# Performance work log

Hardware: AMD Instinct MI355X
Metric: run time of the kernel (lower is better)

Reference implementation:

```python
import jax, jax.numpy as jnp
import numpy as np

K, S = 8, 4  # patch kernel and stride (overlapping: stride < kernel)


def _patch_idx(H, W):
    nH = (H - K) // S + 1
    nW = (W - K) // S + 1
    hh = (jnp.arange(nH) * S)[:, None] + jnp.arange(K)[None, :]  # [nH, K]
    ww = (jnp.arange(nW) * S)[:, None] + jnp.arange(K)[None, :]  # [nW, K]
    return nH, nW, hh, ww


def _split(x):
    # x: [B, C, H, W] -> [B*N, K*K, C] (same token/patch ordering as nn.Unfold)
    B, C, H, W = x.shape
    nH, nW, hh, ww = _patch_idx(H, W)
    # gather overlapping patches: [B, C, nH, nW, K, K]
    p = x[:, :, hh[:, None, :, None], ww[None, :, None, :]]
    p = jnp.transpose(p, (0, 2, 3, 4, 5, 1))  # [B, nH, nW, K, K, C]
    return p.reshape(B * nH * nW, K * K, C)


def _merge(z, B, C, H, W):
    # z: [B*N, K*K, C] -> overlap-add fold -> [B, C, H, W] (matches nn.Fold)
    nH, nW, hh, ww = _patch_idx(H, W)
    y = z.reshape(B, nH, nW, K, K, C)
    y = jnp.transpose(y, (0, 5, 1, 2, 3, 4))  # [B, C, nH, nW, K, K]
    out = jnp.zeros((B, C, H, W), z.dtype)
    out = out.at[:, :, hh[:, None, :, None], ww[None, :, None, :]].add(y)
    return out


def reference(q, k, v):
    B, C, H, W = v.shape
    qp = _split(q)  # [BN, KK, C]
    kp = _split(k)
    vp = _split(v)
    scale = C ** (-0.5)
    # per-patch attention over KK=64 tokens
    attn = jax.nn.softmax(scale * jnp.einsum('ntc,nsc->nts', qp, kp), axis=-1)
    z = jnp.einsum('nts,nsc->ntc', attn, vp)  # [BN, KK, C]
    return _merge(z, B, C, H, W)


def setup_inputs() -> dict:
    key = jax.random.key(0)
    k1, k2, k3 = jax.random.split(key, 3)
    shape = (8, 128, 128, 128)  # [B, C, H, W]
    return {
        'q': jax.random.normal(k1, shape, dtype=jnp.float32),
        'k': jax.random.normal(k2, shape, dtype=jnp.float32),
        'v': jax.random.normal(k3, shape, dtype=jnp.float32),
    }
```

## Files before the change

### kernel.cpp

```cpp
#include <hip/hip_runtime.h>

#define B_    8
#define C_    128
#define H_    128
#define W_    128
#define NH    31
#define NPB   (NH*NH)
#define NPAT  (B_*NPB)
#define HW_   (H_*W_)
#define CHW_  (C_*HW_)
#define WS_BYTES ((size_t)NPAT * 8192 * 2)

typedef float v4f __attribute__((ext_vector_type(4)));
typedef short v8s __attribute__((ext_vector_type(8)));

__device__ __forceinline__ unsigned short f2bf(float f) {
    unsigned int u = __builtin_bit_cast(unsigned int, f);
    u += 0x7FFFu + ((u >> 16) & 1u);
    return (unsigned short)(u >> 16);
}
__device__ __forceinline__ float bflo(unsigned int d) {
    return __builtin_bit_cast(float, d << 16);
}
__device__ __forceinline__ float bfhi(unsigned int d) {
    return __builtin_bit_cast(float, d & 0xFFFF0000u);
}


__global__ __launch_bounds__(512, 6)
void patch_attn_ws(const float* __restrict__ q,
                   const float* __restrict__ k,
                   const float* __restrict__ v,
                   unsigned short* __restrict__ ws)
{
    __shared__ __align__(16) unsigned char lds[43264];
    unsigned short* sQ   = (unsigned short*)(lds);
    unsigned short* sK   = (unsigned short*)(lds + 16384);
    unsigned short* sVT  = (unsigned short*)(lds);
    unsigned short* sP   = (unsigned short*)(lds + 32768);
    float*          sRedM= (float*)(lds + 40960);
    float*          sRedL= (float*)(lds + 41984);
    float*          sInv = (float*)(lds + 43008);
    unsigned short* sRep = (unsigned short*)(lds);

    const int tid  = threadIdx.x;
    const int lane = tid & 63;
    const int wid  = tid >> 6;
    const int l15  = lane & 15;
    const int quad = lane >> 4;

    const int p   = (blockIdx.x & 7) * NPB + (blockIdx.x >> 3);
    const int b   = p / NPB;
    const int rem = p - b * NPB;
    const int ph  = rem / NH;
    const int pw  = rem - ph * NH;
    const int h0  = ph * 4, w0 = pw * 4;
    const int baseB = b * CHW_;

    float4 rq[4], rk[4], rv[4];
    int cA[4], tA[4];
    #pragma unroll
    for (int g = 0; g < 4; ++g) {
        int flat4 = tid + g * 512;
        int jj = flat4 & 1;
        int i  = (flat4 >> 1) & 7;
        int c  = flat4 >> 4;
        int off = baseB + c * HW_ + (h0 + i) * W_ + (w0 + jj * 4);
        rq[g] = *(const float4*)(q + off);
        rk[g] = *(const float4*)(k + off);
        rv[g] = *(const float4*)(v + off);
        cA[g] = c;
        tA[g] = i * 8 + jj * 4;
    }
    #pragma unroll
    for (int g = 0; g < 4; ++g) {
        const float* fq = (const float*)&rq[g];
        const float* fk = (const float*)&rk[g];
        int c = cA[g];
        #pragma unroll
        for (int d = 0; d < 4; ++d) {
            int t = tA[g] + d;
            int idx = t * 128 + ((((c >> 3) ^ (t & 15)) << 3) | (c & 7));
            sQ[idx] = f2bf(fq[d]);
            sK[idx] = f2bf(fk[d]);
        }
    }
    __syncthreads();

    const float scale = 0.08838834764831845f;
    const int nt  = wid & 3;
    const int mt0 = wid >> 2;

    v4f accT[2];
    #pragma unroll
    for (int ti = 0; ti < 2; ++ti) {
        int mt = mt0 + ti * 2;
        v4f acc = {0.f, 0.f, 0.f, 0.f};
        int rowA = mt * 16 + l15;
        int rowB = nt * 16 + l15;
        #pragma unroll
        for (int kk = 0; kk < 4; ++kk) {
            int gph = (kk * 4 + quad) ^ l15;
            v8s a  = *(const v8s*)(&sQ[rowA * 128 + gph * 8]);
            v8s bb = *(const v8s*)(&sK[rowB * 128 + gph * 8]);
            acc = __builtin_amdgcn_mfma_f32_16x16x32_bf16(a, bb, acc, 0, 0, 0);
        }
        #pragma unroll
        for (int r = 0; r < 4; ++r) acc[r] *= scale;
        accT[ti] = acc;
    }

    float4 mloc[2], eV[2];
    #pragma unroll
    for (int ti = 0; ti < 2; ++ti) {
        float4 m;
        #pragma unroll
        for (int r = 0; r < 4; ++r) m[r] = accT[ti][r];
        #pragma unroll
        for (int mask = 1; mask <= 8; mask <<= 1)
            #pragma unroll
            for (int r = 0; r < 4; ++r) m[r] = fmaxf(m[r], __shfl_xor(m[r], mask));
        float4 e, l;
        #pragma unroll
        for (int r = 0; r < 4; ++r) { e[r] = __expf(accT[ti][r] - m[r]); l[r] = e[r]; }
        #pragma unroll
        for (int mask = 1; mask <= 8; mask <<= 1)
            #pragma unroll
            for (int r = 0; r < 4; ++r) l[r] += __shfl_xor(l[r], mask);
        mloc[ti] = m; eV[ti] = e;
        if (l15 == 0) {
            int tb = (mt0 + ti * 2) * 16 + quad * 4;
            #pragma unroll
            for (int r = 0; r < 4; ++r) {
                sRedM[nt * 64 + tb + r] = m[r];
                sRedL[nt * 64 + tb + r] = l[r];
            }
        }
    }
    __syncthreads();

    #pragma unroll
    for (int g = 0; g < 4; ++g) {
        const float* fv = (const float*)&rv[g];
        unsigned short tmp[4];
        #pragma unroll
        for (int d = 0; d < 4; ++d) tmp[d] = f2bf(fv[d]);
        int c = cA[g], s0 = tA[g];
        int idx = c * 64 + ((((s0 >> 3) ^ (c & 7)) << 3) | (s0 & 7));
        *(uint2*)(&sVT[idx]) = *(const uint2*)tmp;
    }

    #pragma unroll
    for (int ti = 0; ti < 2; ++ti) {
        int tb = (mt0 + ti * 2) * 16 + quad * 4;
        float4 Mv[4], Lv[4];
        #pragma unroll
        for (int n2 = 0; n2 < 4; ++n2) {
            Mv[n2] = *(const float4*)(&sRedM[n2 * 64 + tb]);
            Lv[n2] = *(const float4*)(&sRedL[n2 * 64 + tb]);
        }
        float4 M = Mv[0], L;
        #pragma unroll
        for (int n2 = 1; n2 < 4; ++n2)
            #pragma unroll
            for (int r = 0; r < 4; ++r) M[r] = fmaxf(M[r], Mv[n2][r]);
        #pragma unroll
        for (int r = 0; r < 4; ++r) L[r] = 0.f;
        #pragma unroll
        for (int n2 = 0; n2 < 4; ++n2)
            #pragma unroll
            for (int r = 0; r < 4; ++r) L[r] += Lv[n2][r] * __expf(Mv[n2][r] - M[r]);
        #pragma unroll
        for (int r = 0; r < 4; ++r) {
            float pv = eV[ti][r] * __expf(mloc[ti][r] - M[r]);
            int t = tb + r;
            int s = nt * 16 + l15;
            sP[t * 64 + ((((s >> 3) ^ (t & 7)) << 3) | (s & 7))] = f2bf(pv);
        }
        if (nt == 0 && l15 == 0) {
            #pragma unroll
            for (int r = 0; r < 4; ++r) sInv[tb + r] = 1.0f / L[r];
        }
    }
    __syncthreads();

    v4f z[4];
    #pragma unroll
    for (int n2 = 0; n2 < 4; ++n2) z[n2] = (v4f){0.f, 0.f, 0.f, 0.f};
    const int crow = wid * 16 + l15;
    #pragma unroll
    for (int kk = 0; kk < 2; ++kk) {
        int gph = (kk * 4 + quad) ^ (l15 & 7);
        v8s a = *(const v8s*)(&sVT[crow * 64 + gph * 8]);
        #pragma unroll
        for (int n2 = 0; n2 < 4; ++n2) {
            int trow = n2 * 16 + l15;
            v8s bb = *(const v8s*)(&sP[trow * 64 + gph * 8]);
            z[n2] = __builtin_amdgcn_mfma_f32_16x16x32_bf16(a, bb, z[n2], 0, 0, 0);
        }
    }
    __syncthreads();

    #pragma unroll
    for (int n2 = 0; n2 < 4; ++n2) {
        int t = n2 * 16 + l15;
        float inv = sInv[t];
        #pragma unroll
        for (int r = 0; r < 4; ++r) {
            int c = wid * 16 + quad * 4 + r;
            sRep[c * 70 + t] = f2bf(z[n2][r] * inv);
        }
    }
    __syncthreads();
    {
        int c = tid >> 2, tseg = tid & 3;
        const unsigned short* src = &sRep[c * 70 + tseg * 16];
        uint2 d0 = *(const uint2*)(src);
        uint2 d1 = *(const uint2*)(src + 4);
        uint2 d2 = *(const uint2*)(src + 8);
        uint2 d3 = *(const uint2*)(src + 12);
        unsigned short* dst = ws + (size_t)p * 8192 + c * 64 + tseg * 16;
        uint4 w0v; w0v.x = d0.x; w0v.y = d0.y; w0v.z = d1.x; w0v.w = d1.y;
        uint4 w1v; w1v.x = d2.x; w1v.y = d2.y; w1v.z = d3.x; w1v.w = d3.y;
        ((uint4*)dst)[0] = w0v;
        ((uint4*)dst)[1] = w1v;
    }
}


#define MSLOT 264
#define MARR  (33 * MSLOT)

__global__ __launch_bounds__(256, 4)
void merge_kernel(const unsigned short* __restrict__ ws,
                  float* __restrict__ out)
{
    __shared__ __align__(16) unsigned short sM[2 * MARR];
    unsigned short* sA = sM;
    unsigned short* sB = sM + MARR;

    const int tid  = threadIdx.x;
    const int b    = blockIdx.x & 7;
    const int rest = blockIdx.x >> 3;
    const int hq   = rest >> 4;
    const int cg   = rest & 15;

    if (tid < 132) {
        int target = tid / 33;
        int j      = tid - target * 33;
        unsigned short* base = ((target < 2) ? sA : sB)
                             + ((target & 1) ? 32 * MSLOT : 0);
        uint4 zz; zz.x = 0u; zz.y = 0u; zz.z = 0u; zz.w = 0u;
        *(uint4*)(base + j * 8) = zz;
    }

    const int aValid = (hq <= 30);
    const int bValid = (hq >= 1);
    const int hqB = bValid ? (hq - 1) : 0;
    const size_t rowA = (size_t)(b * NPB + hq  * NH) * 8192;
    const size_t rowB = (size_t)(b * NPB + hqB * NH) * 8192;

    #pragma unroll
    for (int it = 0; it < 8; ++it) {
        int flat = tid + it * 256;
        if (flat < 1984) {
            int half = (flat >= 992);
            int fl   = flat - (half ? 992 : 0);
            int seg  = fl >> 2;
            int sub  = fl & 3;
            int pw   = seg >> 3;
            int csub = seg & 7;
            const unsigned short* src = ws
                + (half ? rowB : rowA)
                + (size_t)pw * 8192
                + (size_t)(cg * 8 + csub) * 64
                + (half ? 32 : 0)
                + sub * 8;
            int valid = half ? bValid : aValid;
            uint4 val;
            if (valid) {
                val = *(const uint4*)src;
            } else {
                val.x = 0u; val.y = 0u; val.z = 0u; val.w = 0u;
            }
            unsigned short* dst = (half ? sB : sA)
                + (pw + 1) * MSLOT + csub * 32 + sub * 8;
            *(uint4*)dst = val;
        }
    }
    __syncthreads();

    const int l    = tid & 31;
    const int csub = tid >> 5;
    const int c    = cg * 8 + csub;

    float* op = out + b * CHW_ + c * HW_ + (hq * 4) * W_ + l * 4;
    #pragma unroll
    for (int hr = 0; hr < 4; ++hr) {
        int baseL = (l + 1) * MSLOT + csub * 32 + hr * 8;
        int baseP = l       * MSLOT + csub * 32 + hr * 8 + 4;
        uint2 aL = *(const uint2*)(sA + baseL);
        uint2 aP = *(const uint2*)(sA + baseP);
        uint2 bL = *(const uint2*)(sB + baseL);
        uint2 bP = *(const uint2*)(sB + baseP);
        float4 r;
        r.x = bflo(aL.x) + bflo(aP.x) + bflo(bL.x) + bflo(bP.x);
        r.y = bfhi(aL.x) + bfhi(aP.x) + bfhi(bL.x) + bfhi(bP.x);
        r.z = bflo(aL.y) + bflo(aP.y) + bflo(bL.y) + bflo(bP.y);
        r.w = bfhi(aL.y) + bfhi(aP.y) + bfhi(bL.y) + bfhi(bP.y);
        *(float4*)(op + hr * W_) = r;
    }
}


__global__ __launch_bounds__(512, 6)
void patch_attn_atomic(const float* __restrict__ q,
                       const float* __restrict__ k,
                       const float* __restrict__ v,
                       float* __restrict__ out)
{
    __shared__ __align__(16) unsigned char lds[43264];
    unsigned short* sQ   = (unsigned short*)(lds);
    unsigned short* sK   = (unsigned short*)(lds + 16384);
    unsigned short* sVT  = (unsigned short*)(lds);
    unsigned short* sP   = (unsigned short*)(lds + 32768);
    float*          sRedM= (float*)(lds + 40960);
    float*          sRedL= (float*)(lds + 41984);
    float*          sInv = (float*)(lds + 43008);

    const int tid  = threadIdx.x;
    const int lane = tid & 63;
    const int wid  = tid >> 6;
    const int l15  = lane & 15;
    const int quad = lane >> 4;

    const int p   = (blockIdx.x & 7) * NPB + (blockIdx.x >> 3);
    const int b   = p / NPB;
    const int rem = p - b * NPB;
    const int ph  = rem / NH;
    const int pw  = rem - ph * NH;
    const int h0  = ph * 4, w0 = pw * 4;
    const int baseB = b * CHW_;

    float4 rq[4], rk[4], rv[4];
    int cA[4], tA[4];
    #pragma unroll
    for (int g = 0; g < 4; ++g) {
        int flat4 = tid + g * 512;
        int jj = flat4 & 1;
        int i  = (flat4 >> 1) & 7;
        int c  = flat4 >> 4;
        int off = baseB + c * HW_ + (h0 + i) * W_ + (w0 + jj * 4);
        rq[g] = *(const float4*)(q + off);
        rk[g] = *(const float4*)(k + off);
        rv[g] = *(const float4*)(v + off);
        cA[g] = c;
        tA[g] = i * 8 + jj * 4;
    }
    #pragma unroll
    for (int g = 0; g < 4; ++g) {
        const float* fq = (const float*)&rq[g];
        const float* fk = (const float*)&rk[g];
        int c = cA[g];
        #pragma unroll
        for (int d = 0; d < 4; ++d) {
            int t = tA[g] + d;
            int idx = t * 128 + ((((c >> 3) ^ (t & 15)) << 3) | (c & 7));
            sQ[idx] = f2bf(fq[d]);
            sK[idx] = f2bf(fk[d]);
        }
    }
    __syncthreads();

    const float scale = 0.08838834764831845f;
    const int nt  = wid & 3;
    const int mt0 = wid >> 2;

    v4f accT[2];
    #pragma unroll
    for (int ti = 0; ti < 2; ++ti) {
        int mt = mt0 + ti * 2;
        v4f acc = {0.f, 0.f, 0.f, 0.f};
        int rowA = mt * 16 + l15;
        int rowB = nt * 16 + l15;
        #pragma unroll
        for (int kk = 0; kk < 4; ++kk) {
            int gph = (kk * 4 + quad) ^ l15;
            v8s a  = *(const v8s*)(&sQ[rowA * 128 + gph * 8]);
            v8s bb = *(const v8s*)(&sK[rowB * 128 + gph * 8]);
            acc = __builtin_amdgcn_mfma_f32_16x16x32_bf16(a, bb, acc, 0, 0, 0);
        }
        #pragma unroll
        for (int r = 0; r < 4; ++r) acc[r] *= scale;
        accT[ti] = acc;
    }

    float4 mloc[2], eV[2];
    #pragma unroll
    for (int ti = 0; ti < 2; ++ti) {
        float4 m;
        #pragma unroll
        for (int r = 0; r < 4; ++r) m[r] = accT[ti][r];
        #pragma unroll
        for (int mask = 1; mask <= 8; mask <<= 1)
            #pragma unroll
            for (int r = 0; r < 4; ++r) m[r] = fmaxf(m[r], __shfl_xor(m[r], mask));
        float4 e, l;
        #pragma unroll
        for (int r = 0; r < 4; ++r) { e[r] = __expf(accT[ti][r] - m[r]); l[r] = e[r]; }
        #pragma unroll
        for (int mask = 1; mask <= 8; mask <<= 1)
            #pragma unroll
            for (int r = 0; r < 4; ++r) l[r] += __shfl_xor(l[r], mask);
        mloc[ti] = m; eV[ti] = e;
        if (l15 == 0) {
            int tb = (mt0 + ti * 2) * 16 + quad * 4;
            #pragma unroll
            for (int r = 0; r < 4; ++r) {
                sRedM[nt * 64 + tb + r] = m[r];
                sRedL[nt * 64 + tb + r] = l[r];
            }
        }
    }
    __syncthreads();

    #pragma unroll
    for (int g = 0; g < 4; ++g) {
        const float* fv = (const float*)&rv[g];
        unsigned short tmp[4];
        #pragma unroll
        for (int d = 0; d < 4; ++d) tmp[d] = f2bf(fv[d]);
        int c = cA[g], s0 = tA[g];
        int idx = c * 64 + ((((s0 >> 3) ^ (c & 7)) << 3) | (s0 & 7));
        *(uint2*)(&sVT[idx]) = *(const uint2*)tmp;
    }

    #pragma unroll
    for (int ti = 0; ti < 2; ++ti) {
        int tb = (mt0 + ti * 2) * 16 + quad * 4;
        float4 Mv[4], Lv[4];
        #pragma unroll
        for (int n2 = 0; n2 < 4; ++n2) {
            Mv[n2] = *(const float4*)(&sRedM[n2 * 64 + tb]);
            Lv[n2] = *(const float4*)(&sRedL[n2 * 64 + tb]);
        }
        float4 M = Mv[0], L;
        #pragma unroll
        for (int n2 = 1; n2 < 4; ++n2)
            #pragma unroll
            for (int r = 0; r < 4; ++r) M[r] = fmaxf(M[r], Mv[n2][r]);
        #pragma unroll
        for (int r = 0; r < 4; ++r) L[r] = 0.f;
        #pragma unroll
        for (int n2 = 0; n2 < 4; ++n2)
            #pragma unroll
            for (int r = 0; r < 4; ++r) L[r] += Lv[n2][r] * __expf(Mv[n2][r] - M[r]);
        #pragma unroll
        for (int r = 0; r < 4; ++r) {
            float pv = eV[ti][r] * __expf(mloc[ti][r] - M[r]);
            int t = tb + r;
            int s = nt * 16 + l15;
            sP[t * 64 + ((((s >> 3) ^ (t & 7)) << 3) | (s & 7))] = f2bf(pv);
        }
        if (nt == 0 && l15 == 0) {
            #pragma unroll
            for (int r = 0; r < 4; ++r) sInv[tb + r] = 1.0f / L[r];
        }
    }
    __syncthreads();

    v4f z[4];
    #pragma unroll
    for (int n2 = 0; n2 < 4; ++n2) z[n2] = (v4f){0.f, 0.f, 0.f, 0.f};
    const int crow = wid * 16 + l15;
    #pragma unroll
    for (int kk = 0; kk < 2; ++kk) {
        int gph = (kk * 4 + quad) ^ (l15 & 7);
        v8s a = *(const v8s*)(&sVT[crow * 64 + gph * 8]);
        #pragma unroll
        for (int n2 = 0; n2 < 4; ++n2) {
            int trow = n2 * 16 + l15;
            v8s bb = *(const v8s*)(&sP[trow * 64 + gph * 8]);
            z[n2] = __builtin_amdgcn_mfma_f32_16x16x32_bf16(a, bb, z[n2], 0, 0, 0);
        }
    }

    #pragma unroll
    for (int n2 = 0; n2 < 4; ++n2) {
        int t = n2 * 16 + l15;
        float inv = sInv[t];
        int base2 = baseB + (h0 + (t >> 3)) * W_ + (w0 + (t & 7));
        #pragma unroll
        for (int r = 0; r < 4; ++r) {
            int c = wid * 16 + quad * 4 + r;
            unsafeAtomicAdd(out + base2 + c * HW_, z[n2][r] * inv);
        }
    }
}

extern "C" void kernel_launch(void* const* d_in, const int* in_sizes, int n_in,
                              void* d_out, int out_size, void* d_ws, size_t ws_size,
                              hipStream_t stream) {
    const float* q = (const float*)d_in[0];
    const float* k = (const float*)d_in[1];
    const float* v = (const float*)d_in[2];
    float* out = (float*)d_out;

    if (ws_size >= WS_BYTES) {
        unsigned short* ws = (unsigned short*)d_ws;
        patch_attn_ws<<<NPAT, 512, 0, stream>>>(q, k, v, ws);
        merge_kernel<<<8 * 32 * 16, 256, 0, stream>>>(ws, out);
    } else {
        hipMemsetAsync(out, 0, (size_t)out_size * sizeof(float), stream);
        patch_attn_atomic<<<NPAT, 512, 0, stream>>>(q, k, v, out);
    }
}
```

Baseline: 350.2 us.

## Restructure patch attention to 4 waves with in-wave softmax and smaller LDS

```diff
diff --git a/kernel.cpp b/kernel.cpp
--- a/kernel.cpp
+++ b/kernel.cpp
@@ -19,6 +19,9 @@
     u += 0x7FFFu + ((u >> 16) & 1u);
     return (unsigned short)(u >> 16);
 }
+__device__ __forceinline__ unsigned int pack2bf(float lo, float hi) {
+    return (unsigned int)f2bf(lo) | ((unsigned int)f2bf(hi) << 16);
+}
 __device__ __forceinline__ float bflo(unsigned int d) {
     return __builtin_bit_cast(float, d << 16);
 }
@@ -27,27 +30,24 @@
 }
 
 
-__global__ __launch_bounds__(512, 6)
+__global__ __launch_bounds__(256, 4)
 void patch_attn_ws(const float* __restrict__ q,
                    const float* __restrict__ k,
                    const float* __restrict__ v,
                    unsigned short* __restrict__ ws)
 {
-    __shared__ __align__(16) unsigned char lds[43264];
-    unsigned short* sQ   = (unsigned short*)(lds);
-    unsigned short* sK   = (unsigned short*)(lds + 16384);
-    unsigned short* sVT  = (unsigned short*)(lds);
-    unsigned short* sP   = (unsigned short*)(lds + 32768);
-    float*          sRedM= (float*)(lds + 40960);
-    float*          sRedL= (float*)(lds + 41984);
-    float*          sInv = (float*)(lds + 43008);
-    unsigned short* sRep = (unsigned short*)(lds);
+    __shared__ __align__(16) unsigned char lds[32768];
+    unsigned short* sQ  = (unsigned short*)(lds);
+    unsigned short* sK  = (unsigned short*)(lds + 16384);
+    unsigned short* sVT = (unsigned short*)(lds);
+    unsigned short* sP  = (unsigned short*)(lds + 16384);
+    unsigned short* sRep= (unsigned short*)(lds);
 
     const int tid  = threadIdx.x;
     const int lane = tid & 63;
-    const int wid  = tid >> 6;
     const int l15  = lane & 15;
     const int quad = lane >> 4;
+    const int wid  = tid >> 6;
 
     const int p   = (blockIdx.x & 7) * NPB + (blockIdx.x >> 3);
     const int b   = p / NPB;
@@ -57,173 +57,194 @@
     const int h0  = ph * 4, w0 = pw * 4;
     const int baseB = b * CHW_;
 
-    float4 rq[4], rk[4], rv[4];
-    int cA[4], tA[4];
-    #pragma unroll
-    for (int g = 0; g < 4; ++g) {
-        int flat4 = tid + g * 512;
+    {
+        float4 qa[4], qb[4], ka[4], kb[4];
+        int c0A[4], tA[4];
+        #pragma unroll
+        for (int g = 0; g < 4; ++g) {
+            int flat2 = tid + g * 256;
+            int jj = flat2 & 1;
+            int i  = (flat2 >> 1) & 7;
+            int cp = flat2 >> 4;
+            int c0 = cp * 2;
+            int off0 = baseB + c0 * HW_ + (h0 + i) * W_ + (w0 + jj * 4);
+            qa[g] = *(const float4*)(q + off0);
+            qb[g] = *(const float4*)(q + off0 + HW_);
+            ka[g] = *(const float4*)(k + off0);
+            kb[g] = *(const float4*)(k + off0 + HW_);
+            c0A[g] = c0;
+            tA[g]  = i * 8 + jj * 4;
+        }
+        #pragma unroll
+        for (int g = 0; g < 4; ++g) {
+            const float* fqa = (const float*)&qa[g];
+            const float* fqb = (const float*)&qb[g];
+            const float* fka = (const float*)&ka[g];
+            const float* fkb = (const float*)&kb[g];
+            int c0 = c0A[g];
+            #pragma unroll
+            for (int d = 0; d < 4; ++d) {
+                int t = tA[g] + d;
+                int chunk = (c0 >> 3) ^ (t & 15);
+                int pos = t * 128 + chunk * 8 + (c0 & 7);
+                *(unsigned int*)&sQ[pos] = pack2bf(fqa[d], fqb[d]);
+                *(unsigned int*)&sK[pos] = pack2bf(fka[d], fkb[d]);
+            }
+        }
+    }
+    __syncthreads();
+
+    v4f acc0, acc1, acc2, acc3;
+    acc0 = acc1 = acc2 = acc3 = (v4f){0.f, 0.f, 0.f, 0.f};
+    const int rowT = wid * 16 + l15;
+    #pragma unroll
+    for (int kk = 0; kk < 4; ++kk) {
+        int gph = (kk * 4 + quad) ^ l15;
+        v8s bq = *(const v8s*)(&sQ[rowT * 128 + gph * 8]);
+        v8s a0 = *(const v8s*)(&sK[( 0 + l15) * 128 + gph * 8]);
+        v8s a1 = *(const v8s*)(&sK[(16 + l15) * 128 + gph * 8]);
+        v8s a2 = *(const v8s*)(&sK[(32 + l15) * 128 + gph * 8]);
+        v8s a3 = *(const v8s*)(&sK[(48 + l15) * 128 + gph * 8]);
+        acc0 = __builtin_amdgcn_mfma_f32_16x16x32_bf16(a0, bq, acc0, 0, 0, 0);
+        acc1 = __builtin_amdgcn_mfma_f32_16x16x32_bf16(a1, bq, acc1, 0, 0, 0);
+        acc2 = __builtin_amdgcn_mfma_f32_16x16x32_bf16(a2, bq, acc2, 0, 0, 0);
+        acc3 = __builtin_amdgcn_mfma_f32_16x16x32_bf16(a3, bq, acc3, 0, 0, 0);
+    }
+
+    float4 rv[8];
+    int cV[8], sV[8];
+    #pragma unroll
+    for (int g = 0; g < 8; ++g) {
+        int flat4 = tid + g * 256;
         int jj = flat4 & 1;
         int i  = (flat4 >> 1) & 7;
         int c  = flat4 >> 4;
-        int off = baseB + c * HW_ + (h0 + i) * W_ + (w0 + jj * 4);
-        rq[g] = *(const float4*)(q + off);
-        rk[g] = *(const float4*)(k + off);
-        rv[g] = *(const float4*)(v + off);
-        cA[g] = c;
-        tA[g] = i * 8 + jj * 4;
-    }
-    #pragma unroll
-    for (int g = 0; g < 4; ++g) {
-        const float* fq = (const float*)&rq[g];
-        const float* fk = (const float*)&rk[g];
-        int c = cA[g];
-        #pragma unroll
-        for (int d = 0; d < 4; ++d) {
-            int t = tA[g] + d;
-            int idx = t * 128 + ((((c >> 3) ^ (t & 15)) << 3) | (c & 7));
-            sQ[idx] = f2bf(fq[d]);
-            sK[idx] = f2bf(fk[d]);
-        }
-    }
-    __syncthreads();
+        rv[g] = *(const float4*)(v + baseB + c * HW_ + (h0 + i) * W_ + (w0 + jj * 4));
+        cV[g] = c;
+        sV[g] = i * 8 + jj * 4;
+    }
 
     const float scale = 0.08838834764831845f;
-    const int nt  = wid & 3;
-    const int mt0 = wid >> 2;
-
-    v4f accT[2];
-    #pragma unroll
-    for (int ti = 0; ti < 2; ++ti) {
-        int mt = mt0 + ti * 2;
-        v4f acc = {0.f, 0.f, 0.f, 0.f};
-        int rowA = mt * 16 + l15;
-        int rowB = nt * 16 + l15;
-        #pragma unroll
-        for (int kk = 0; kk < 4; ++kk) {
-            int gph = (kk * 4 + quad) ^ l15;
-            v8s a  = *(const v8s*)(&sQ[rowA * 128 + gph * 8]);
-            v8s bb = *(const v8s*)(&sK[rowB * 128 + gph * 8]);
-            acc = __builtin_amdgcn_mfma_f32_16x16x32_bf16(a, bb, acc, 0, 0, 0);
-        }
-        #pragma unroll
-        for (int r = 0; r < 4; ++r) acc[r] *= scale;
-        accT[ti] = acc;
-    }
-
-    float4 mloc[2], eV[2];
-    #pragma unroll
-    for (int ti = 0; ti < 2; ++ti) {
-        float4 m;
-        #pragma unroll
-        for (int r = 0; r < 4; ++r) m[r] = accT[ti][r];
-        #pragma unroll
-        for (int mask = 1; mask <= 8; mask <<= 1)
-            #pragma unroll
-            for (int r = 0; r < 4; ++r) m[r] = fmaxf(m[r], __shfl_xor(m[r], mask));
-        float4 e, l;
-        #pragma unroll
-        for (int r = 0; r < 4; ++r) { e[r] = __expf(accT[ti][r] - m[r]); l[r] = e[r]; }
-        #pragma unroll
-        for (int mask = 1; mask <= 8; mask <<= 1)
-            #pragma unroll
-            for (int r = 0; r < 4; ++r) l[r] += __shfl_xor(l[r], mask);
-        mloc[ti] = m; eV[ti] = e;
-        if (l15 == 0) {
-            int tb = (mt0 + ti * 2) * 16 + quad * 4;
-            #pragma unroll
-            for (int r = 0; r < 4; ++r) {
-                sRedM[nt * 64 + tb + r] = m[r];
-                sRedL[nt * 64 + tb + r] = l[r];
-            }
-        }
-    }
-    __syncthreads();
-
-    #pragma unroll
-    for (int g = 0; g < 4; ++g) {
+    float e0[4], e1[4], e2[4], e3[4];
+    unsigned int pPk[8];
+    {
+        float mx = -1e30f;
+        #pragma unroll
+        for (int r = 0; r < 4; ++r) {
+            e0[r] = acc0[r] * scale; mx = fmaxf(mx, e0[r]);
+            e1[r] = acc1[r] * scale; mx = fmaxf(mx, e1[r]);
+            e2[r] = acc2[r] * scale; mx = fmaxf(mx, e2[r]);
+            e3[r] = acc3[r] * scale; mx = fmaxf(mx, e3[r]);
+        }
+        mx = fmaxf(mx, __shfl_xor(mx, 16));
+        mx = fmaxf(mx, __shfl_xor(mx, 32));
+        float sum = 0.f;
+        #pragma unroll
+        for (int r = 0; r < 4; ++r) {
+            e0[r] = __expf(e0[r] - mx); sum += e0[r];
+            e1[r] = __expf(e1[r] - mx); sum += e1[r];
+            e2[r] = __expf(e2[r] - mx); sum += e2[r];
+            e3[r] = __expf(e3[r] - mx); sum += e3[r];
+        }
+        sum += __shfl_xor(sum, 16);
+        sum += __shfl_xor(sum, 32);
+        float inv = 1.0f / sum;
+        pPk[0] = pack2bf(e0[0] * inv, e0[1] * inv);
+        pPk[1] = pack2bf(e0[2] * inv, e0[3] * inv);
+        pPk[2] = pack2bf(e1[0] * inv, e1[1] * inv);
+        pPk[3] = pack2bf(e1[2] * inv, e1[3] * inv);
+        pPk[4] = pack2bf(e2[0] * inv, e2[1] * inv);
+        pPk[5] = pack2bf(e2[2] * inv, e2[3] * inv);
+        pPk[6] = pack2bf(e3[0] * inv, e3[1] * inv);
+        pPk[7] = pack2bf(e3[2] * inv, e3[3] * inv);
+    }
+    __syncthreads();
+
+    #pragma unroll
+    for (int g = 0; g < 8; ++g) {
         const float* fv = (const float*)&rv[g];
-        unsigned short tmp[4];
-        #pragma unroll
-        for (int d = 0; d < 4; ++d) tmp[d] = f2bf(fv[d]);
-        int c = cA[g], s0 = tA[g];
+        int c = cV[g], s0 = sV[g];
+        unsigned int w0p = pack2bf(fv[0], fv[1]);
+        unsigned int w1p = pack2bf(fv[2], fv[3]);
         int idx = c * 64 + ((((s0 >> 3) ^ (c & 7)) << 3) | (s0 & 7));
-        *(uint2*)(&sVT[idx]) = *(const uint2*)tmp;
-    }
-
-    #pragma unroll
-    for (int ti = 0; ti < 2; ++ti) {
-        int tb = (mt0 + ti * 2) * 16 + quad * 4;
-        float4 Mv[4], Lv[4];
-        #pragma unroll
-        for (int n2 = 0; n2 < 4; ++n2) {
-            Mv[n2] = *(const float4*)(&sRedM[n2 * 64 + tb]);
-            Lv[n2] = *(const float4*)(&sRedL[n2 * 64 + tb]);
-        }
-        float4 M = Mv[0], L;
-        #pragma unroll
-        for (int n2 = 1; n2 < 4; ++n2)
-            #pragma unroll
-            for (int r = 0; r < 4; ++r) M[r] = fmaxf(M[r], Mv[n2][r]);
-        #pragma unroll
-        for (int r = 0; r < 4; ++r) L[r] = 0.f;
-        #pragma unroll
-        for (int n2 = 0; n2 < 4; ++n2)
-            #pragma unroll
-            for (int r = 0; r < 4; ++r) L[r] += Lv[n2][r] * __expf(Mv[n2][r] - M[r]);
-        #pragma unroll
-        for (int r = 0; r < 4; ++r) {
-            float pv = eV[ti][r] * __expf(mloc[ti][r] - M[r]);
-            int t = tb + r;
-            int s = nt * 16 + l15;
-            sP[t * 64 + ((((s >> 3) ^ (t & 7)) << 3) | (s & 7))] = f2bf(pv);
-        }
-        if (nt == 0 && l15 == 0) {
-            #pragma unroll
-            for (int r = 0; r < 4; ++r) sInv[tb + r] = 1.0f / L[r];
-        }
-    }
-    __syncthreads();
-
-    v4f z[4];
-    #pragma unroll
-    for (int n2 = 0; n2 < 4; ++n2) z[n2] = (v4f){0.f, 0.f, 0.f, 0.f};
-    const int crow = wid * 16 + l15;
+        uint2 val; val.x = w0p; val.y = w1p;
+        *(uint2*)(&sVT[idx]) = val;
+    }
+
+    {
+        const int t = rowT;
+        const int qh = quad >> 1, ql = quad & 1;
+        #pragma unroll
+        for (int m = 0; m < 4; ++m) {
+            int chunk = (m * 2 + qh) ^ (t & 7);
+            uint2 val;
+            val.x = pPk[m * 2];
+            val.y = pPk[m * 2 + 1];
+            *(uint2*)(&sP[t * 64 + chunk * 8 + ql * 4]) = val;
+        }
+    }
+    __syncthreads();
+
+    v4f z00, z01, z02, z03, z10, z11, z12, z13;
+    z00 = z01 = z02 = z03 = (v4f){0.f, 0.f, 0.f, 0.f};
+    z10 = z11 = z12 = z13 = (v4f){0.f, 0.f, 0.f, 0.f};
     #pragma unroll
     for (int kk = 0; kk < 2; ++kk) {
         int gph = (kk * 4 + quad) ^ (l15 & 7);
-        v8s a = *(const v8s*)(&sVT[crow * 64 + gph * 8]);
-        #pragma unroll
-        for (int n2 = 0; n2 < 4; ++n2) {
-            int trow = n2 * 16 + l15;
-            v8s bb = *(const v8s*)(&sP[trow * 64 + gph * 8]);
-            z[n2] = __builtin_amdgcn_mfma_f32_16x16x32_bf16(a, bb, z[n2], 0, 0, 0);
-        }
-    }
-    __syncthreads();
-
-    #pragma unroll
-    for (int n2 = 0; n2 < 4; ++n2) {
-        int t = n2 * 16 + l15;
-        float inv = sInv[t];
+        v8s b0 = *(const v8s*)(&sP[( 0 + l15) * 64 + gph * 8]);
+        v8s b1 = *(const v8s*)(&sP[(16 + l15) * 64 + gph * 8]);
+        v8s b2 = *(const v8s*)(&sP[(32 + l15) * 64 + gph * 8]);
+        v8s b3 = *(const v8s*)(&sP[(48 + l15) * 64 + gph * 8]);
+        v8s aA = *(const v8s*)(&sVT[(wid * 32      + l15) * 64 + gph * 8]);
+        v8s aB = *(const v8s*)(&sVT[(wid * 32 + 16 + l15) * 64 + gph * 8]);
+        z00 = __builtin_amdgcn_mfma_f32_16x16x32_bf16(aA, b0, z00, 0, 0, 0);
+        z01 = __builtin_amdgcn_mfma_f32_16x16x32_bf16(aA, b1, z01, 0, 0, 0);
+        z02 = __builtin_amdgcn_mfma_f32_16x16x32_bf16(aA, b2, z02, 0, 0, 0);
+        z03 = __builtin_amdgcn_mfma_f32_16x16x32_bf16(aA, b3, z03, 0, 0, 0);
+        z10 = __builtin_amdgcn_mfma_f32_16x16x32_bf16(aB, b0, z10, 0, 0, 0);
+        z11 = __builtin_amdgcn_mfma_f32_16x16x32_bf16(aB, b1, z11, 0, 0, 0);
+        z12 = __builtin_amdgcn_mfma_f32_16x16x32_bf16(aB, b2, z12, 0, 0, 0);
+        z13 = __builtin_amdgcn_mfma_f32_16x16x32_bf16(aB, b3, z13, 0, 0, 0);
+    }
+    __syncthreads();
+
+    {
+        const int cb0 = wid * 32 + quad * 4;
         #pragma unroll
         for (int r = 0; r < 4; ++r) {
-            int c = wid * 16 + quad * 4 + r;
-            sRep[c * 70 + t] = f2bf(z[n2][r] * inv);
-        }
-    }
-    __syncthreads();
+            int cA = cb0 + r, cB = cb0 + 16 + r;
+            sRep[cA * 66 + ( 0 + l15)] = f2bf(z00[r]);
+            sRep[cA * 66 + (16 + l15)] = f2bf(z01[r]);
+            sRep[cA * 66 + (32 + l15)] = f2bf(z02[r]);
+            sRep[cA * 66 + (48 + l15)] = f2bf(z03[r]);
+            sRep[cB * 66 + ( 0 + l15)] = f2bf(z10[r]);
+            sRep[cB * 66 + (16 + l15)] = f2bf(z11[r]);
+            sRep[cB * 66 + (32 + l15)] = f2bf(z12[r]);
+            sRep[cB * 66 + (48 + l15)] = f2bf(z13[r]);
+        }
+    }
+    __syncthreads();
+
     {
-        int c = tid >> 2, tseg = tid & 3;
-        const unsigned short* src = &sRep[c * 70 + tseg * 16];
+        int c = tid >> 1, th = tid & 1;
+        const unsigned short* src = &sRep[c * 66 + th * 32];
         uint2 d0 = *(const uint2*)(src);
         uint2 d1 = *(const uint2*)(src + 4);
         uint2 d2 = *(const uint2*)(src + 8);
         uint2 d3 = *(const uint2*)(src + 12);
-        unsigned short* dst = ws + (size_t)p * 8192 + c * 64 + tseg * 16;
+        uint2 d4 = *(const uint2*)(src + 16);
+        uint2 d5 = *(const uint2*)(src + 20);
+        uint2 d6 = *(const uint2*)(src + 24);
+        uint2 d7 = *(const uint2*)(src + 28);
+        unsigned short* dst = ws + (size_t)p * 8192 + c * 64 + th * 32;
         uint4 w0v; w0v.x = d0.x; w0v.y = d0.y; w0v.z = d1.x; w0v.w = d1.y;
         uint4 w1v; w1v.x = d2.x; w1v.y = d2.y; w1v.z = d3.x; w1v.w = d3.y;
+        uint4 w2v; w2v.x = d4.x; w2v.y = d4.y; w2v.z = d5.x; w2v.w = d5.y;
+        uint4 w3v; w3v.x = d6.x; w3v.y = d6.y; w3v.z = d7.x; w3v.w = d7.y;
         ((uint4*)dst)[0] = w0v;
         ((uint4*)dst)[1] = w1v;
+        ((uint4*)dst)[2] = w2v;
+        ((uint4*)dst)[3] = w3v;
     }
 }
 
@@ -508,7 +529,7 @@
 
     if (ws_size >= WS_BYTES) {
         unsigned short* ws = (unsigned short*)d_ws;
-        patch_attn_ws<<<NPAT, 512, 0, stream>>>(q, k, v, ws);
+        patch_attn_ws<<<NPAT, 256, 0, stream>>>(q, k, v, ws);
         merge_kernel<<<8 * 32 * 16, 256, 0, stream>>>(ws, out);
     } else {
         hipMemsetAsync(out, 0, (size_t)out_size * sizeof(float), stream);
```

Measured after the change: 347.4 us. Within noise of the previous version (-0.8%).
